# Performance work log

Hardware: AMD Instinct MI355X
Metric: run time of the kernel (lower is better)

Reference implementation:

```python
import jax, jax.numpy as jnp
import numpy as np


def setup_inputs() -> dict:
    key = jax.random.key(0)
    k1, k2 = jax.random.split(key)
    x1 = jax.random.normal(k1, (16, 512, 64, 64), dtype=jnp.float32)
    x2 = jax.random.normal(k2, (16, 512, 64, 64), dtype=jnp.float32)
    return {"x1": x1, "x2": x2}


def reference(x1, x2):
    B, C1, H, W = x1.shape
    C2 = x2.shape[1]
    N = H * W
    x1_d = x1.reshape(B, C1, N)  # (B, C1, N)
    x2_d = x2.reshape(B, C2, N)  # (B, C2, N)
    # energy[b, i, j] = sum_n x1_d[b, i, n] * x2_d[b, j, n]
    energy = jnp.einsum('bin,bjn->bij', x1_d, x2_d)  # (B, C1, C2)
    attention = jax.nn.softmax(energy, axis=-1)       # softmax over C2
    # attention^T @ x1_d -> (B, C2, N)
    attention_value = jnp.einsum('bij,bin->bjn', attention, x1_d).reshape(B, C2, H, W)
    out = jnp.concatenate((x1, attention_value), axis=1)  # (B, C1+C2, H, W)
    return (out, attention)
```

## Files before the change

### kernel.cpp

```cpp
#include <hip/hip_runtime.h>

typedef short bf16x8 __attribute__((ext_vector_type(8)));
typedef float f32x4  __attribute__((ext_vector_type(4)));
typedef unsigned int u32;
typedef unsigned short u16;

#define NBATCH 16
#define C      512
#define NPIX   4096
#define ATT_OFF ((size_t)NBATCH * 1024 * NPIX)

__global__ __launch_bounds__(512, 2) void gemm1_energy(
    const float* __restrict__ x1, const float* __restrict__ x2,
    float* __restrict__ out)
{
    __shared__ __align__(16) u16 smem[2][2][4][128 * 32];

    const int tid  = threadIdx.x;
    const int team = tid >> 8;
    const int ttid = tid & 255;
    const int lane = tid & 63;
    const int w    = (tid >> 6) & 3;
    const int wr   = (w >> 1) * 64;
    const int wc   = (w & 1) * 64;
    const int r16  = lane & 15;
    const int g    = lane >> 4;

    const int gid = (blockIdx.x & 7) * 32 + (blockIdx.x >> 3);
    const int b   = gid >> 4;
    const int ib  = ((gid >> 2) & 3) * 128;
    const int jb  = (gid & 3) * 128;

    const int nr = ttid >> 2;
    const int kq = ttid & 3;
    const int ko = team * 2048;

    const float* Ab = x1 + (size_t)(b * C + ib + nr) * NPIX + ko + kq * 8;
    const float* Bb = x2 + (size_t)(b * C + jb + nr) * NPIX + ko + kq * 8;
    float* cpyA = out + (size_t)(b * 1024 + ib + nr) * NPIX + ko + kq * 8;
    const int csel = jb >> 7;

    f32x4 pa[2][2], pb[2][2];

    auto loadk = [&](int kt) {
        const int off = kt * 32;
        #pragma unroll
        for (int c = 0; c < 2; ++c) {
            pa[c][0] = *(const f32x4*)(Ab + (size_t)c * 64 * NPIX + off);
            pa[c][1] = *(const f32x4*)(Ab + (size_t)c * 64 * NPIX + off + 4);
            pb[c][0] = *(const f32x4*)(Bb + (size_t)c * 64 * NPIX + off);
            pb[c][1] = *(const f32x4*)(Bb + (size_t)c * 64 * NPIX + off + 4);
        }
    };

    auto stage = [&](int kt, int buf) {
        #pragma unroll
        for (int c = 0; c < 2; ++c) {
            const int row = nr + c * 64;
            const u32 sw = (u32)((row * 64 + kq * 16) ^ (((row >> 1) & 3) << 4));
            u32 ahp[4], alp[4], bhp[4], blp[4];
            #pragma unroll
            for (int p = 0; p < 4; ++p) {
                const float fa0 = pa[c][p >> 1][(p & 1) * 2];
                const float fa1 = pa[c][p >> 1][(p & 1) * 2 + 1];
                const u32 ua0 = __float_as_uint(fa0), ua1 = __float_as_uint(fa1);
                const float la0 = fa0 - __uint_as_float(ua0 & 0xFFFF0000u);
                const float la1 = fa1 - __uint_as_float(ua1 & 0xFFFF0000u);
                ahp[p] = __builtin_amdgcn_perm(ua1, ua0, 0x07060302u);
                alp[p] = __builtin_amdgcn_perm(__float_as_uint(la1), __float_as_uint(la0), 0x07060302u);
                const float fb0 = pb[c][p >> 1][(p & 1) * 2];
                const float fb1 = pb[c][p >> 1][(p & 1) * 2 + 1];
                const u32 ub0 = __float_as_uint(fb0), ub1 = __float_as_uint(fb1);
                const float lb0 = fb0 - __uint_as_float(ub0 & 0xFFFF0000u);
                const float lb1 = fb1 - __uint_as_float(ub1 & 0xFFFF0000u);
                bhp[p] = __builtin_amdgcn_perm(ub1, ub0, 0x07060302u);
                blp[p] = __builtin_amdgcn_perm(__float_as_uint(lb1), __float_as_uint(lb0), 0x07060302u);
            }
            *(uint4*)((char*)smem[team][buf][0] + sw) = make_uint4(ahp[0], ahp[1], ahp[2], ahp[3]);
            *(uint4*)((char*)smem[team][buf][1] + sw) = make_uint4(alp[0], alp[1], alp[2], alp[3]);
            *(uint4*)((char*)smem[team][buf][2] + sw) = make_uint4(bhp[0], bhp[1], bhp[2], bhp[3]);
            *(uint4*)((char*)smem[team][buf][3] + sw) = make_uint4(blp[0], blp[1], blp[2], blp[3]);
            if ((row >> 5) == csel) {
                *(f32x4*)(cpyA + (size_t)c * 64 * NPIX + kt * 32)     = pa[c][0];
                *(f32x4*)(cpyA + (size_t)c * 64 * NPIX + kt * 32 + 4) = pa[c][1];
            }
        }
    };

    const f32x4 zero4 = {0.f, 0.f, 0.f, 0.f};
    f32x4 acc[4][4];
    #pragma unroll
    for (int i = 0; i < 4; ++i)
        #pragma unroll
        for (int j = 0; j < 4; ++j) acc[i][j] = zero4;

    loadk(0);
    stage(0, 0);

    for (int kt = 0; kt < 64; ++kt) {
        if (kt < 63) loadk(kt + 1);
        __syncthreads();
        const int buf = kt & 1;

        bf16x8 ah[4], al[4], bh[4], bl[4];
        #pragma unroll
        for (int f = 0; f < 4; ++f) {
            const int ar = wr + f * 16 + r16;
            const u32 ao = (u32)((ar * 64 + g * 16) ^ (((ar >> 1) & 3) << 4));
            ah[f] = *(const bf16x8*)((const char*)smem[team][buf][0] + ao);
            al[f] = *(const bf16x8*)((const char*)smem[team][buf][1] + ao);
            const int br = wc + f * 16 + r16;
            const u32 bo = (u32)((br * 64 + g * 16) ^ (((br >> 1) & 3) << 4));
            bh[f] = *(const bf16x8*)((const char*)smem[team][buf][2] + bo);
            bl[f] = *(const bf16x8*)((const char*)smem[team][buf][3] + bo);
        }
        #pragma unroll
        for (int fi = 0; fi < 4; ++fi)
            #pragma unroll
            for (int fj = 0; fj < 4; ++fj) {
                acc[fi][fj] = __builtin_amdgcn_mfma_f32_16x16x32_bf16(ah[fi], bh[fj], acc[fi][fj], 0, 0, 0);
                acc[fi][fj] = __builtin_amdgcn_mfma_f32_16x16x32_bf16(ah[fi], bl[fj], acc[fi][fj], 0, 0, 0);
                acc[fi][fj] = __builtin_amdgcn_mfma_f32_16x16x32_bf16(al[fi], bh[fj], acc[fi][fj], 0, 0, 0);
            }
        if (kt < 63) stage(kt + 1, buf ^ 1);
    }

    __syncthreads();
    f32x4* red = (f32x4*)&smem[0][0][0][0];
    const int slot = w * 64 + lane;
    if (team == 1) {
        #pragma unroll
        for (int c = 0; c < 16; ++c) red[c * 256 + slot] = acc[c >> 2][c & 3];
    }
    __syncthreads();
    if (team == 0) {
        float* att = out + ATT_OFF + (size_t)b * C * C;
        #pragma unroll
        for (int fi = 0; fi < 4; ++fi)
            #pragma unroll
            for (int fj = 0; fj < 4; ++fj) {
                f32x4 v = acc[fi][fj];
                const f32x4 o = red[(fi * 4 + fj) * 256 + slot];
                const int j = jb + wc + fj * 16 + r16;
                #pragma unroll
                for (int q = 0; q < 4; ++q) {
                    const int i = ib + wr + fi * 16 + g * 4 + q;
                    att[(size_t)i * C + j] = v[q] + o[q];
                }
            }
    }
}

__global__ __launch_bounds__(256) void softmax_rows(float* __restrict__ att)
{
    float* p = att + (size_t)blockIdx.x * C;
    const int t = threadIdx.x;
    const int lane = t & 63, wid = t >> 6;
    __shared__ float red[8];

    float a = p[t], c = p[t + 256];
    float m = fmaxf(a, c);
    #pragma unroll
    for (int o = 32; o; o >>= 1) m = fmaxf(m, __shfl_xor(m, o));
    if (lane == 0) red[wid] = m;
    __syncthreads();
    m = fmaxf(fmaxf(red[0], red[1]), fmaxf(red[2], red[3]));

    float e0 = __expf(a - m), e1 = __expf(c - m);
    float s = e0 + e1;
    #pragma unroll
    for (int o = 32; o; o >>= 1) s += __shfl_xor(s, o);
    if (lane == 0) red[4 + wid] = s;
    __syncthreads();
    s = (red[4] + red[5]) + (red[6] + red[7]);
    const float inv = 1.0f / s;
    p[t]       = e0 * inv;
    p[t + 256] = e1 * inv;
}

#define KST 36

__global__ __launch_bounds__(256, 3) void gemm2_av(
    const float* __restrict__ x1, float* __restrict__ out)
{
    __shared__ __align__(16) u16 Aj[2][128 * KST];
    __shared__ __align__(16) u16 Bn[2][128 * KST];

    const float* att = out + ATT_OFF;
    const int tid  = threadIdx.x;
    const int lane = tid & 63;
    const int wid  = tid >> 6;
    const int wr   = (wid >> 1) * 64;
    const int wc   = (wid & 1) * 64;
    const int r16  = lane & 15;
    const int g    = lane >> 4;

    const int gid = (blockIdx.x & 7) * 256 + (blockIdx.x >> 3);
    const int b   = gid >> 7;
    const int jt  = (gid >> 5) & 3;
    const int nt  = gid & 31;
    const int jb  = jt * 128;
    const int nb  = nt * 128;

    const int col = (tid & 31) * 4;
    const int ks  = (tid >> 5) * 4;

    const float* ap0 = att + (size_t)b * C * C    + (size_t)ks * C    + jb + col;
    const float* bp0 = x1  + (size_t)b * C * NPIX + (size_t)ks * NPIX + nb + col;

    u32 sa[8], sb[8];

    auto loadpack = [&](int kt) {
        f32x4 L[4];
        #pragma unroll
        for (int i = 0; i < 4; ++i) L[i] = *(const f32x4*)(ap0 + (size_t)(kt * 32 + i) * C);
        #pragma unroll
        for (int jj = 0; jj < 4; ++jj) {
            sa[jj * 2]     = __builtin_amdgcn_perm(__float_as_uint(L[1][jj]), __float_as_uint(L[0][jj]), 0x07060302u);
            sa[jj * 2 + 1] = __builtin_amdgcn_perm(__float_as_uint(L[3][jj]), __float_as_uint(L[2][jj]), 0x07060302u);
        }
        #pragma unroll
        for (int i = 0; i < 4; ++i) L[i] = *(const f32x4*)(bp0 + (size_t)(kt * 32 + i) * NPIX);
        #pragma unroll
        for (int jj = 0; jj < 4; ++jj) {
            sb[jj * 2]     = __builtin_amdgcn_perm(__float_as_uint(L[1][jj]), __float_as_uint(L[0][jj]), 0x07060302u);
            sb[jj * 2 + 1] = __builtin_amdgcn_perm(__float_as_uint(L[3][jj]), __float_as_uint(L[2][jj]), 0x07060302u);
        }
    };

    auto stage = [&](int buf) {
        #pragma unroll
        for (int jj = 0; jj < 4; ++jj) {
            *(uint2*)((char*)Aj[buf] + ((col + jj) * KST + ks) * 2) = make_uint2(sa[jj * 2], sa[jj * 2 + 1]);
            *(uint2*)((char*)Bn[buf] + ((col + jj) * KST + ks) * 2) = make_uint2(sb[jj * 2], sb[jj * 2 + 1]);
        }
    };

    const f32x4 zero4 = {0.f, 0.f, 0.f, 0.f};
    f32x4 acc[4][4];
    #pragma unroll
    for (int i = 0; i < 4; ++i)
        #pragma unroll
        for (int j = 0; j < 4; ++j) acc[i][j] = zero4;

    loadpack(0);
    stage(0);

    for (int kt = 0; kt < 16; ++kt) {
        if (kt < 15) loadpack(kt + 1);
        __syncthreads();
        const int buf = kt & 1;

        union { bf16x8 v; uint2 u2[2]; } fa[4], fb[4];
        #pragma unroll
        for (int f = 0; f < 4; ++f) {
            const int aj = wr + f * 16 + r16;
            fa[f].u2[0] = *(const uint2*)(&Aj[buf][aj * KST + g * 8]);
            fa[f].u2[1] = *(const uint2*)(&Aj[buf][aj * KST + g * 8 + 4]);
            const int bn = wc + f * 16 + r16;
            fb[f].u2[0] = *(const uint2*)(&Bn[buf][bn * KST + g * 8]);
            fb[f].u2[1] = *(const uint2*)(&Bn[buf][bn * KST + g * 8 + 4]);
        }
        #pragma unroll
        for (int fi = 0; fi < 4; ++fi)
            #pragma unroll
            for (int fj = 0; fj < 4; ++fj)
                acc[fi][fj] = __builtin_amdgcn_mfma_f32_16x16x32_bf16(fa[fi].v, fb[fj].v, acc[fi][fj], 0, 0, 0);
        if (kt < 15) stage(buf ^ 1);
    }

    #pragma unroll
    for (int fi = 0; fi < 4; ++fi)
        #pragma unroll
        for (int fj = 0; fj < 4; ++fj) {
            const int n = nb + wc + fj * 16 + r16;
            #pragma unroll
            for (int q = 0; q < 4; ++q) {
                const int j = jb + wr + fi * 16 + g * 4 + q;
                out[(size_t)(b * 1024 + 512 + j) * NPIX + n] = acc[fi][fj][q];
            }
        }
}

extern "C" void kernel_launch(void* const* d_in, const int* in_sizes, int n_in,
                              void* d_out, int out_size, void* d_ws, size_t ws_size,
                              hipStream_t stream) {
    const float* x1 = (const float*)d_in[0];
    const float* x2 = (const float*)d_in[1];
    float* out = (float*)d_out;
    (void)in_sizes; (void)n_in; (void)out_size; (void)d_ws; (void)ws_size;

    gemm1_energy<<<dim3(256),  dim3(512), 0, stream>>>(x1, x2, out);
    softmax_rows<<<dim3(8192), dim3(256), 0, stream>>>(out + ATT_OFF);
    gemm2_av    <<<dim3(2048), dim3(256), 0, stream>>>(x1, out);
}
```

Measured before the change: 272.9 us.

## Split-K energy GEMM across blocks with direct global-to-LDS loads

The energy GEMM now uses 512 blocks of 256 threads, each computing half the K range, instead of two intra-block teams that reduced through shared memory. The second K-half partial is written into the not-yet-filled attention_value region of the output and summed inside the softmax kernel. Tiles are brought in as raw fp32 via global_load_lds with an XOR swizzle, and the bf16 hi/lo split moves to after the LDS read. The x1 copy into the concatenated output moves from GEMM1 to GEMM2, and MFMA sections get raised wave priority. Costs include doubled LDS footprint per tile, redundant split work per wave, and extra partial-sum traffic through global memory.

```diff
diff --git a/kernel.cpp b/kernel.cpp
--- a/kernel.cpp
+++ b/kernel.cpp
@@ -10,80 +10,58 @@
 #define NPIX   4096
 #define ATT_OFF ((size_t)NBATCH * 1024 * NPIX)
 
-__global__ __launch_bounds__(512, 2) void gemm1_energy(
+typedef __attribute__((address_space(1))) const u32* gp_t;
+typedef __attribute__((address_space(3))) u32* lp_t;
+
+__device__ __forceinline__ void splitpair(u32 u0, u32 u1, u32& h, u32& l) {
+    h = __builtin_amdgcn_perm(u1, u0, 0x07060302u);
+    const u32 m0 = u0 & 0xFFFF0000u, m1 = u1 & 0xFFFF0000u;
+    const float l0 = __uint_as_float(u0) - __uint_as_float(m0);
+    const float l1 = __uint_as_float(u1) - __uint_as_float(m1);
+    l = __builtin_amdgcn_perm(__float_as_uint(l1), __float_as_uint(l0), 0x07060302u);
+}
+
+__global__ __launch_bounds__(256, 2) void gemm1_energy(
     const float* __restrict__ x1, const float* __restrict__ x2,
     float* __restrict__ out)
 {
-    __shared__ __align__(16) u16 smem[2][2][4][128 * 32];
+    __shared__ __align__(16) float Asm[2][128 * 32];
+    __shared__ __align__(16) float Bsm[2][128 * 32];
 
     const int tid  = threadIdx.x;
-    const int team = tid >> 8;
-    const int ttid = tid & 255;
     const int lane = tid & 63;
-    const int w    = (tid >> 6) & 3;
+    const int w    = tid >> 6;
     const int wr   = (w >> 1) * 64;
     const int wc   = (w & 1) * 64;
     const int r16  = lane & 15;
     const int g    = lane >> 4;
 
-    const int gid = (blockIdx.x & 7) * 32 + (blockIdx.x >> 3);
-    const int b   = gid >> 4;
-    const int ib  = ((gid >> 2) & 3) * 128;
-    const int jb  = (gid & 3) * 128;
-
-    const int nr = ttid >> 2;
-    const int kq = ttid & 3;
-    const int ko = team * 2048;
-
-    const float* Ab = x1 + (size_t)(b * C + ib + nr) * NPIX + ko + kq * 8;
-    const float* Bb = x2 + (size_t)(b * C + jb + nr) * NPIX + ko + kq * 8;
-    float* cpyA = out + (size_t)(b * 1024 + ib + nr) * NPIX + ko + kq * 8;
-    const int csel = jb >> 7;
-
-    f32x4 pa[2][2], pb[2][2];
-
-    auto loadk = [&](int kt) {
-        const int off = kt * 32;
-        #pragma unroll
-        for (int c = 0; c < 2; ++c) {
-            pa[c][0] = *(const f32x4*)(Ab + (size_t)c * 64 * NPIX + off);
-            pa[c][1] = *(const f32x4*)(Ab + (size_t)c * 64 * NPIX + off + 4);
-            pb[c][0] = *(const f32x4*)(Bb + (size_t)c * 64 * NPIX + off);
-            pb[c][1] = *(const f32x4*)(Bb + (size_t)c * 64 * NPIX + off + 4);
-        }
-    };
+    const int gid = (blockIdx.x & 7) * 64 + (blockIdx.x >> 3);
+    const int b   = gid >> 5;
+    const int ib  = ((gid >> 3) & 3) * 128;
+    const int jb  = ((gid >> 1) & 3) * 128;
+    const int ks  = gid & 1;
+    const int ko  = ks * 2048;
+
+    const int lrow  = lane >> 3;
+    const int chunk = lane & 7;
+    const float* srcA[4];
+    const float* srcB[4];
+    #pragma unroll
+    for (int q = 0; q < 4; ++q) {
+        const int row = w * 32 + q * 8 + lrow;
+        const int sc  = (chunk ^ ((row >> 1) & 7)) * 4;
+        srcA[q] = x1 + (size_t)(b * C + ib + row) * NPIX + ko + sc;
+        srcB[q] = x2 + (size_t)(b * C + jb + row) * NPIX + ko + sc;
+    }
 
     auto stage = [&](int kt, int buf) {
         #pragma unroll
-        for (int c = 0; c < 2; ++c) {
-            const int row = nr + c * 64;
-            const u32 sw = (u32)((row * 64 + kq * 16) ^ (((row >> 1) & 3) << 4));
-            u32 ahp[4], alp[4], bhp[4], blp[4];
-            #pragma unroll
-            for (int p = 0; p < 4; ++p) {
-                const float fa0 = pa[c][p >> 1][(p & 1) * 2];
-                const float fa1 = pa[c][p >> 1][(p & 1) * 2 + 1];
-                const u32 ua0 = __float_as_uint(fa0), ua1 = __float_as_uint(fa1);
-                const float la0 = fa0 - __uint_as_float(ua0 & 0xFFFF0000u);
-                const float la1 = fa1 - __uint_as_float(ua1 & 0xFFFF0000u);
-                ahp[p] = __builtin_amdgcn_perm(ua1, ua0, 0x07060302u);
-                alp[p] = __builtin_amdgcn_perm(__float_as_uint(la1), __float_as_uint(la0), 0x07060302u);
-                const float fb0 = pb[c][p >> 1][(p & 1) * 2];
-                const float fb1 = pb[c][p >> 1][(p & 1) * 2 + 1];
-                const u32 ub0 = __float_as_uint(fb0), ub1 = __float_as_uint(fb1);
-                const float lb0 = fb0 - __uint_as_float(ub0 & 0xFFFF0000u);
-                const float lb1 = fb1 - __uint_as_float(ub1 & 0xFFFF0000u);
-                bhp[p] = __builtin_amdgcn_perm(ub1, ub0, 0x07060302u);
-                blp[p] = __builtin_amdgcn_perm(__float_as_uint(lb1), __float_as_uint(lb0), 0x07060302u);
-            }
-            *(uint4*)((char*)smem[team][buf][0] + sw) = make_uint4(ahp[0], ahp[1], ahp[2], ahp[3]);
-            *(uint4*)((char*)smem[team][buf][1] + sw) = make_uint4(alp[0], alp[1], alp[2], alp[3]);
-            *(uint4*)((char*)smem[team][buf][2] + sw) = make_uint4(bhp[0], bhp[1], bhp[2], bhp[3]);
-            *(uint4*)((char*)smem[team][buf][3] + sw) = make_uint4(blp[0], blp[1], blp[2], blp[3]);
-            if ((row >> 5) == csel) {
-                *(f32x4*)(cpyA + (size_t)c * 64 * NPIX + kt * 32)     = pa[c][0];
-                *(f32x4*)(cpyA + (size_t)c * 64 * NPIX + kt * 32 + 4) = pa[c][1];
-            }
+        for (int q = 0; q < 4; ++q) {
+            __builtin_amdgcn_global_load_lds((gp_t)(const void*)(srcA[q] + kt * 32),
+                                             (lp_t)(void*)&Asm[buf][(w * 32 + q * 8) * 32], 16, 0, 0);
+            __builtin_amdgcn_global_load_lds((gp_t)(const void*)(srcB[q] + kt * 32),
+                                             (lp_t)(void*)&Bsm[buf][(w * 32 + q * 8) * 32], 16, 0, 0);
         }
     };
 
@@ -94,71 +72,82 @@
         #pragma unroll
         for (int j = 0; j < 4; ++j) acc[i][j] = zero4;
 
-    loadk(0);
+    union B8 { bf16x8 v; u32 u[4]; };
+
     stage(0, 0);
 
     for (int kt = 0; kt < 64; ++kt) {
-        if (kt < 63) loadk(kt + 1);
+        const int buf = kt & 1;
         __syncthreads();
-        const int buf = kt & 1;
-
-        bf16x8 ah[4], al[4], bh[4], bl[4];
+
+        B8 ah[4], al[4], bh[4], bl[4];
+        uint4 UA[4][2], UB[4][2];
         #pragma unroll
         for (int f = 0; f < 4; ++f) {
             const int ar = wr + f * 16 + r16;
-            const u32 ao = (u32)((ar * 64 + g * 16) ^ (((ar >> 1) & 3) << 4));
-            ah[f] = *(const bf16x8*)((const char*)smem[team][buf][0] + ao);
-            al[f] = *(const bf16x8*)((const char*)smem[team][buf][1] + ao);
+            const float* abase = &Asm[buf][ar * 32];
+            UA[f][0] = *(const uint4*)(abase + (((2 * g)     ^ ((ar >> 1) & 7)) * 4));
+            UA[f][1] = *(const uint4*)(abase + (((2 * g + 1) ^ ((ar >> 1) & 7)) * 4));
             const int br = wc + f * 16 + r16;
-            const u32 bo = (u32)((br * 64 + g * 16) ^ (((br >> 1) & 3) << 4));
-            bh[f] = *(const bf16x8*)((const char*)smem[team][buf][2] + bo);
-            bl[f] = *(const bf16x8*)((const char*)smem[team][buf][3] + bo);
-        }
+            const float* bbase = &Bsm[buf][br * 32];
+            UB[f][0] = *(const uint4*)(bbase + (((2 * g)     ^ ((br >> 1) & 7)) * 4));
+            UB[f][1] = *(const uint4*)(bbase + (((2 * g + 1) ^ ((br >> 1) & 7)) * 4));
+        }
+        if (kt < 63) stage(kt + 1, buf ^ 1);
+
+        #pragma unroll
+        for (int f = 0; f < 4; ++f) {
+            splitpair(UA[f][0].x, UA[f][0].y, ah[f].u[0], al[f].u[0]);
+            splitpair(UA[f][0].z, UA[f][0].w, ah[f].u[1], al[f].u[1]);
+            splitpair(UA[f][1].x, UA[f][1].y, ah[f].u[2], al[f].u[2]);
+            splitpair(UA[f][1].z, UA[f][1].w, ah[f].u[3], al[f].u[3]);
+            splitpair(UB[f][0].x, UB[f][0].y, bh[f].u[0], bl[f].u[0]);
+            splitpair(UB[f][0].z, UB[f][0].w, bh[f].u[1], bl[f].u[1]);
+            splitpair(UB[f][1].x, UB[f][1].y, bh[f].u[2], bl[f].u[2]);
+            splitpair(UB[f][1].z, UB[f][1].w, bh[f].u[3], bl[f].u[3]);
+        }
+
+        __builtin_amdgcn_s_setprio(1);
         #pragma unroll
         for (int fi = 0; fi < 4; ++fi)
             #pragma unroll
             for (int fj = 0; fj < 4; ++fj) {
-                acc[fi][fj] = __builtin_amdgcn_mfma_f32_16x16x32_bf16(ah[fi], bh[fj], acc[fi][fj], 0, 0, 0);
-                acc[fi][fj] = __builtin_amdgcn_mfma_f32_16x16x32_bf16(ah[fi], bl[fj], acc[fi][fj], 0, 0, 0);
-                acc[fi][fj] = __builtin_amdgcn_mfma_f32_16x16x32_bf16(al[fi], bh[fj], acc[fi][fj], 0, 0, 0);
+                acc[fi][fj] = __builtin_amdgcn_mfma_f32_16x16x32_bf16(ah[fi].v, bh[fj].v, acc[fi][fj], 0, 0, 0);
+                acc[fi][fj] = __builtin_amdgcn_mfma_f32_16x16x32_bf16(ah[fi].v, bl[fj].v, acc[fi][fj], 0, 0, 0);
+                acc[fi][fj] = __builtin_amdgcn_mfma_f32_16x16x32_bf16(al[fi].v, bh[fj].v, acc[fi][fj], 0, 0, 0);
             }
-        if (kt < 63) stage(kt + 1, buf ^ 1);
+        __builtin_amdgcn_s_setprio(0);
     }
 
-    __syncthreads();
-    f32x4* red = (f32x4*)&smem[0][0][0][0];
-    const int slot = w * 64 + lane;
-    if (team == 1) {
-        #pragma unroll
-        for (int c = 0; c < 16; ++c) red[c * 256 + slot] = acc[c >> 2][c & 3];
-    }
-    __syncthreads();
-    if (team == 0) {
-        float* att = out + ATT_OFF + (size_t)b * C * C;
-        #pragma unroll
-        for (int fi = 0; fi < 4; ++fi)
-            #pragma unroll
-            for (int fj = 0; fj < 4; ++fj) {
-                f32x4 v = acc[fi][fj];
-                const f32x4 o = red[(fi * 4 + fj) * 256 + slot];
-                const int j = jb + wc + fj * 16 + r16;
-                #pragma unroll
-                for (int q = 0; q < 4; ++q) {
-                    const int i = ib + wr + fi * 16 + g * 4 + q;
-                    att[(size_t)i * C + j] = v[q] + o[q];
-                }
+    float* dst = (ks == 0) ? (out + ATT_OFF + (size_t)b * C * C)
+                           : (out + (size_t)(b * 1024 + 512) * NPIX);
+    #pragma unroll
+    for (int fi = 0; fi < 4; ++fi)
+        #pragma unroll
+        for (int fj = 0; fj < 4; ++fj) {
+            const int j = jb + wc + fj * 16 + r16;
+            #pragma unroll
+            for (int q = 0; q < 4; ++q) {
+                const int i = ib + wr + fi * 16 + g * 4 + q;
+                dst[(size_t)i * C + j] = acc[fi][fj][q];
             }
-    }
-}
-
-__global__ __launch_bounds__(256) void softmax_rows(float* __restrict__ att)
+        }
+}
+
+__global__ __launch_bounds__(256) void softmax_rows(float* __restrict__ out)
 {
-    float* p = att + (size_t)blockIdx.x * C;
+    const int bi = blockIdx.x;
+    const int b  = bi >> 9;
+    const int i  = bi & 511;
+    float* p        = out + ATT_OFF + (size_t)bi * C;
+    const float* pk = out + (size_t)(b * 1024 + 512) * NPIX + (size_t)i * C;
+
     const int t = threadIdx.x;
     const int lane = t & 63, wid = t >> 6;
     __shared__ float red[8];
 
-    float a = p[t], c = p[t + 256];
+    float a = p[t] + pk[t];
+    float c = p[t + 256] + pk[t + 256];
     float m = fmaxf(a, c);
     #pragma unroll
     for (int o = 32; o; o >>= 1) m = fmaxf(m, __shfl_xor(m, o));
@@ -203,36 +192,40 @@
     const int nb  = nt * 128;
 
     const int col = (tid & 31) * 4;
-    const int ks  = (tid >> 5) * 4;
-
-    const float* ap0 = att + (size_t)b * C * C    + (size_t)ks * C    + jb + col;
-    const float* bp0 = x1  + (size_t)b * C * NPIX + (size_t)ks * NPIX + nb + col;
-
-    u32 sa[8], sb[8];
-
-    auto loadpack = [&](int kt) {
-        f32x4 L[4];
-        #pragma unroll
-        for (int i = 0; i < 4; ++i) L[i] = *(const f32x4*)(ap0 + (size_t)(kt * 32 + i) * C);
+    const int ksr = (tid >> 5) * 4;
+
+    const float* ap0 = att + (size_t)b * C * C    + (size_t)ksr * C    + jb + col;
+    const float* bp0 = x1  + (size_t)b * C * NPIX + (size_t)ksr * NPIX + nb + col;
+    float* cpy = out + (size_t)(b * 1024 + ksr) * NPIX + nb + col;
+
+    f32x4 La[4], Lb[4];
+
+    auto loadk = [&](int kt) {
+        #pragma unroll
+        for (int i = 0; i < 4; ++i) {
+            La[i] = *(const f32x4*)(ap0 + (size_t)(kt * 32 + i) * C);
+            Lb[i] = *(const f32x4*)(bp0 + (size_t)(kt * 32 + i) * NPIX);
+        }
+    };
+
+    auto stage = [&](int kt, int buf) {
+        u32 sa[8], sb[8];
         #pragma unroll
         for (int jj = 0; jj < 4; ++jj) {
-            sa[jj * 2]     = __builtin_amdgcn_perm(__float_as_uint(L[1][jj]), __float_as_uint(L[0][jj]), 0x07060302u);
-            sa[jj * 2 + 1] = __builtin_amdgcn_perm(__float_as_uint(L[3][jj]), __float_as_uint(L[2][jj]), 0x07060302u);
-        }
-        #pragma unroll
-        for (int i = 0; i < 4; ++i) L[i] = *(const f32x4*)(bp0 + (size_t)(kt * 32 + i) * NPIX);
+            sa[jj * 2]     = __builtin_amdgcn_perm(__float_as_uint(La[1][jj]), __float_as_uint(La[0][jj]), 0x07060302u);
+            sa[jj * 2 + 1] = __builtin_amdgcn_perm(__float_as_uint(La[3][jj]), __float_as_uint(La[2][jj]), 0x07060302u);
+            sb[jj * 2]     = __builtin_amdgcn_perm(__float_as_uint(Lb[1][jj]), __float_as_uint(Lb[0][jj]), 0x07060302u);
+            sb[jj * 2 + 1] = __builtin_amdgcn_perm(__float_as_uint(Lb[3][jj]), __float_as_uint(Lb[2][jj]), 0x07060302u);
+        }
         #pragma unroll
         for (int jj = 0; jj < 4; ++jj) {
-            sb[jj * 2]     = __builtin_amdgcn_perm(__float_as_uint(L[1][jj]), __float_as_uint(L[0][jj]), 0x07060302u);
-            sb[jj * 2 + 1] = __builtin_amdgcn_perm(__float_as_uint(L[3][jj]), __float_as_uint(L[2][jj]), 0x07060302u);
-        }
-    };
-
-    auto stage = [&](int buf) {
-        #pragma unroll
-        for (int jj = 0; jj < 4; ++jj) {
-            *(uint2*)((char*)Aj[buf] + ((col + jj) * KST + ks) * 2) = make_uint2(sa[jj * 2], sa[jj * 2 + 1]);
-            *(uint2*)((char*)Bn[buf] + ((col + jj) * KST + ks) * 2) = make_uint2(sb[jj * 2], sb[jj * 2 + 1]);
+            *(uint2*)((char*)Aj[buf] + ((col + jj) * KST + ksr) * 2) = make_uint2(sa[jj * 2], sa[jj * 2 + 1]);
+            *(uint2*)((char*)Bn[buf] + ((col + jj) * KST + ksr) * 2) = make_uint2(sb[jj * 2], sb[jj * 2 + 1]);
+        }
+        if (jt == 0) {
+            #pragma unroll
+            for (int i = 0; i < 4; ++i)
+                *(f32x4*)(cpy + (size_t)(kt * 32 + i) * NPIX) = Lb[i];
         }
     };
 
@@ -243,11 +236,11 @@
         #pragma unroll
         for (int j = 0; j < 4; ++j) acc[i][j] = zero4;
 
-    loadpack(0);
-    stage(0);
+    loadk(0);
+    stage(0, 0);
 
     for (int kt = 0; kt < 16; ++kt) {
-        if (kt < 15) loadpack(kt + 1);
+        if (kt < 15) loadk(kt + 1);
         __syncthreads();
         const int buf = kt & 1;
 
@@ -261,12 +254,14 @@
             fb[f].u2[0] = *(const uint2*)(&Bn[buf][bn * KST + g * 8]);
             fb[f].u2[1] = *(const uint2*)(&Bn[buf][bn * KST + g * 8 + 4]);
         }
+        __builtin_amdgcn_s_setprio(1);
         #pragma unroll
         for (int fi = 0; fi < 4; ++fi)
             #pragma unroll
             for (int fj = 0; fj < 4; ++fj)
                 acc[fi][fj] = __builtin_amdgcn_mfma_f32_16x16x32_bf16(fa[fi].v, fb[fj].v, acc[fi][fj], 0, 0, 0);
-        if (kt < 15) stage(buf ^ 1);
+        __builtin_amdgcn_s_setprio(0);
+        if (kt < 15) stage(kt + 1, buf ^ 1);
     }
 
     #pragma unroll
@@ -290,7 +285,7 @@
     float* out = (float*)d_out;
     (void)in_sizes; (void)n_in; (void)out_size; (void)d_ws; (void)ws_size;
 
-    gemm1_energy<<<dim3(256),  dim3(512), 0, stream>>>(x1, x2, out);
-    softmax_rows<<<dim3(8192), dim3(256), 0, stream>>>(out + ATT_OFF);
+    gemm1_energy<<<dim3(512),  dim3(256), 0, stream>>>(x1, x2, out);
+    softmax_rows<<<dim3(8192), dim3(256), 0, stream>>>(out);
     gemm2_av    <<<dim3(2048), dim3(256), 0, stream>>>(x1, out);
 }
```

Measured after the change: 235.0 us. -13.9%, faster.
